# Kernel optimization log

Measured on AMD Instinct MI355X. Metric: run time of the kernel, lower is better.

Reference implementation:

```python
import jax, jax.numpy as jnp
import numpy as np

B, S, D, H = 4, 1024, 1024, 16
DK = D // H
NEG = -1e9


def setup_inputs() -> dict:
    key = jax.random.key(0)
    ks = jax.random.split(key, 8)
    inp = {
        "query": jax.random.normal(ks[0], (B, S, D), dtype=jnp.float32),
        "key": jax.random.normal(ks[1], (B, S, D), dtype=jnp.float32),
        "value": jax.random.normal(ks[2], (B, S, D), dtype=jnp.float32),
        "mask": jax.random.randint(ks[3], (B, S, S), 0, 2, dtype=jnp.int32),
        # bias-free Linear weights, torch layout [out, in]; y = x @ W.T
        "Wq": jax.random.normal(ks[4], (D, D), dtype=jnp.float32) / np.sqrt(D),
        "Wk": jax.random.normal(ks[5], (D, D), dtype=jnp.float32) / np.sqrt(D),
        "Wv": jax.random.normal(ks[6], (D, D), dtype=jnp.float32) / np.sqrt(D),
        "Wo": jax.random.normal(ks[7], (D, D), dtype=jnp.float32) / np.sqrt(D),
    }
    return inp


def _split_heads(x):
    # [B, S, D] -> [B, H, S, DK]
    return x.reshape(B, -1, H, DK).transpose(0, 2, 1, 3)


def reference(query, key, value, mask, Wq, Wk, Wv, Wo):
    q = _split_heads(query @ Wq.T)
    k = _split_heads(key @ Wk.T)
    v = _split_heads(value @ Wv.T)
    scores = jnp.einsum("bhqd,bhkd->bhqk", q, k) / jnp.sqrt(jnp.float32(DK))
    scores = jnp.where(mask[:, None, :, :] == 0, NEG, scores)
    p_attn = jax.nn.softmax(scores, axis=-1)
    x = jnp.einsum("bhqk,bhkd->bhqd", p_attn, v)
    x = x.transpose(0, 2, 1, 3).reshape(B, -1, D)
    # dropout p=0.0 (eval-equivalent): identity
    return x @ Wo.T
```

## Files before the change

### kernel.cpp

```cpp
#include <hip/hip_runtime.h>

#define BB 4
#define SS 1024
#define DD 1024
#define HH 16
#define DKK 64
#define MM (BB*SS)

typedef __bf16 bf16;
typedef __bf16 bf16x8 __attribute__((ext_vector_type(8)));
typedef float f32x4 __attribute__((ext_vector_type(4)));
typedef float f32x16 __attribute__((ext_vector_type(16)));

__device__ __forceinline__ f32x4 mfma16(bf16x8 a, bf16x8 b, f32x4 c) {
  return __builtin_amdgcn_mfma_f32_16x16x32_bf16(a, b, c, 0, 0, 0);
}
__device__ __forceinline__ f32x16 mfma32(bf16x8 a, bf16x8 b, f32x16 c) {
  return __builtin_amdgcn_mfma_f32_32x32x16_bf16(a, b, c, 0, 0, 0);
}
__device__ __forceinline__ float fexp2(float x) {
  return __builtin_amdgcn_exp2f(x);
}
__device__ __forceinline__ void gld_lds16(const bf16* g, bf16* l) {
  __builtin_amdgcn_global_load_lds(
      (const __attribute__((address_space(1))) void*)g,
      (__attribute__((address_space(3))) void*)l, 16, 0, 0);
}

__global__ __launch_bounds__(256)
void k_cvt7(const float* __restrict__ s0, const float* __restrict__ s1,
            const float* __restrict__ s2, const float* __restrict__ s3,
            const float* __restrict__ s4, const float* __restrict__ s5,
            const float* __restrict__ s6,
            bf16* __restrict__ d0, bf16* __restrict__ d1, bf16* __restrict__ d2,
            bf16* __restrict__ d3, bf16* __restrict__ d4, bf16* __restrict__ d5,
            bf16* __restrict__ d6) {
  const int t = blockIdx.y;
  const float* s = (t == 0) ? s0 : (t == 1) ? s1 : (t == 2) ? s2
                 : (t == 3) ? s3 : (t == 4) ? s4 : (t == 5) ? s5 : s6;
  bf16* d = (t == 0) ? d0 : (t == 1) ? d1 : (t == 2) ? d2
          : (t == 3) ? d3 : (t == 4) ? d4 : (t == 5) ? d5 : d6;
  const int n = (t < 3) ? (MM * DD) : (DD * DD);
  const int i0 = (blockIdx.x * 256 + threadIdx.x) * 8;
  if (i0 >= n) return;
  const f32x4 a = *(const f32x4*)(s + i0);
  const f32x4 b = *(const f32x4*)(s + i0 + 4);
  bf16x8 o;
#pragma unroll
  for (int j = 0; j < 4; ++j) { o[j] = (bf16)a[j]; o[4 + j] = (bf16)b[j]; }
  *(bf16x8*)(d + i0) = o;
}

__global__ __launch_bounds__(256) void k_mask_bits(const int* __restrict__ mask,
                                                   unsigned* __restrict__ bits) {
  const int row = blockIdx.x;
  const int b = row >> 10, q = row & 1023;
  const int qblk = q >> 6, qt = (q >> 5) & 1, l = q & 31;
  const size_t base = ((size_t)(b * 16 + qblk) * 2 + qt) * 4;
  const int tid = threadIdx.x;
  const int lane = tid & 63, wv = tid >> 6;
#pragma unroll
  for (int it = 0; it < 4; ++it) {
    const int cb = it * 256 + wv * 64;
    unsigned long long bal = __ballot(mask[(size_t)row * SS + cb + lane] != 0);
    if (lane == 0) {
      const int c0 = cb >> 5;
#pragma unroll
      for (int dd = 0; dd < 2; ++dd) {
        const int c = c0 + dd;
        bits[((base + (c >> 3)) * 8 + (c & 7)) * 32 + l] =
            (unsigned)(bal >> (32 * dd));
      }
    }
  }
}

__global__ __launch_bounds__(256)
void k_kfrag(const bf16* __restrict__ K, bf16* __restrict__ Kf) {
  __shared__ bf16 Kl[32 * 66];
  const int kvb = blockIdx.x, h = blockIdx.y, b = blockIdx.z;
  const int tid = threadIdx.x;
  const int r = tid >> 3, c0 = (tid & 7) * 8;
  *(bf16x8*)&Kl[r * 66 + c0] =
      *(const bf16x8*)(K + (size_t)(b * SS + kvb * 32 + r) * DD + h * 64 + c0);
  __syncthreads();
  const int lane = tid & 63, l31 = lane & 31, hi = lane >> 5;
  const int kt = tid >> 6;
  bf16x8 ok;
#pragma unroll
  for (int j = 0; j < 8; ++j) ok[j] = Kl[l31 * 66 + kt * 16 + hi * 8 + j];
  *(bf16x8*)(Kf + ((size_t)((b * HH + h) * 32 + kvb)) * 2048 + tid * 8) = ok;
}

#define QSCALE 0.1803368801111204f

template<int AF32, int CF32>
__device__ __forceinline__ void gemm_body(const void* __restrict__ Ap,
                                          const float* __restrict__ Wp,
                                          void* __restrict__ Cp,
                                          int Mtot, int N, int K, int blk,
                                          float oscale) {
  __shared__ bf16 Al[128 * 40];
  __shared__ bf16 Bl[128 * 40];
  const int tid = threadIdx.x;
  const int lane = tid & 63;
  const int l15 = lane & 15, l4 = lane >> 4;
  const int wv = tid >> 6;
  const int nbm = Mtot >> 7;
  const int bm = blk % nbm, bn = blk / nbm;
  const size_t m0 = (size_t)bm << 7, n0 = (size_t)bn << 7;
  const int wr = (wv >> 1) << 6, wc = (wv & 1) << 6;
  const int srow = tid >> 2, scol = (tid & 3) << 3;

  f32x4 acc[4][4];
#pragma unroll
  for (int i = 0; i < 4; ++i)
#pragma unroll
    for (int j = 0; j < 4; ++j) acc[i][j] = f32x4{0.f, 0.f, 0.f, 0.f};

  for (int k0 = 0; k0 < K; k0 += 32) {
#pragma unroll
    for (int c = 0; c < 2; ++c) {
      const int row = (c << 6) + srow;
      bf16x8 av;
      if (AF32) {
        const float* s = (const float*)Ap + (m0 + row) * (size_t)K + k0 + scol;
        f32x4 v0 = *(const f32x4*)s;
        f32x4 v1 = *(const f32x4*)(s + 4);
#pragma unroll
        for (int j = 0; j < 4; ++j) { av[j] = (bf16)v0[j]; av[4 + j] = (bf16)v1[j]; }
      } else {
        av = *(const bf16x8*)((const bf16*)Ap + (m0 + row) * (size_t)K + k0 + scol);
      }
      *(bf16x8*)&Al[row * 40 + scol] = av;

      const float* ws_ = Wp + (n0 + row) * (size_t)K + k0 + scol;
      f32x4 w0 = *(const f32x4*)ws_;
      f32x4 w1 = *(const f32x4*)(ws_ + 4);
      bf16x8 wv8;
#pragma unroll
      for (int j = 0; j < 4; ++j) { wv8[j] = (bf16)w0[j]; wv8[4 + j] = (bf16)w1[j]; }
      *(bf16x8*)&Bl[row * 40 + scol] = wv8;
    }
    __syncthreads();

    bf16x8 af[4], bfv[4];
#pragma unroll
    for (int t = 0; t < 4; ++t) {
      af[t]  = *(const bf16x8*)&Al[(wr + t * 16 + l15) * 40 + l4 * 8];
      bfv[t] = *(const bf16x8*)&Bl[(wc + t * 16 + l15) * 40 + l4 * 8];
    }
    __builtin_amdgcn_s_setprio(1);
#pragma unroll
    for (int mt = 0; mt < 4; ++mt)
#pragma unroll
      for (int nt = 0; nt < 4; ++nt)
        acc[mt][nt] = mfma16(af[mt], bfv[nt], acc[mt][nt]);
    __builtin_amdgcn_s_setprio(0);
    __syncthreads();
  }

#pragma unroll
  for (int mt = 0; mt < 4; ++mt)
#pragma unroll
    for (int nt = 0; nt < 4; ++nt)
#pragma unroll
      for (int r = 0; r < 4; ++r) {
        const size_t row = m0 + wr + mt * 16 + l4 * 4 + r;
        const size_t col = n0 + wc + nt * 16 + l15;
        if (CF32) ((float*)Cp)[row * N + col] = acc[mt][nt][r];
        else      ((bf16*)Cp)[row * N + col] = (bf16)(acc[mt][nt][r] * oscale);
      }
}

__global__ __launch_bounds__(256)
void k_gemm_qkv(const float* __restrict__ A0, const float* __restrict__ A1,
                const float* __restrict__ A2, const float* __restrict__ W0,
                const float* __restrict__ W1, const float* __restrict__ W2,
                bf16* __restrict__ C0, bf16* __restrict__ C1, bf16* __restrict__ C2) {
  const int z = blockIdx.z;
  const float* A = (z == 0) ? A0 : (z == 1) ? A1 : A2;
  const float* W = (z == 0) ? W0 : (z == 1) ? W1 : W2;
  bf16* C = (z == 0) ? C0 : (z == 1) ? C1 : C2;
  const float sc = (z == 0) ? QSCALE : 1.0f;
  gemm_body<1, 0>(A, W, C, MM, DD, DD, blockIdx.x, sc);
}

__global__ __launch_bounds__(256)
void k_gemm_out(const bf16* __restrict__ A, const float* __restrict__ W,
                float* __restrict__ C) {
  gemm_body<0, 1>(A, W, C, MM, DD, DD, blockIdx.x, 1.0f);
}

__global__ __launch_bounds__(256)
void k_gemm_qkv_b16(const bf16* __restrict__ A0, const bf16* __restrict__ A1,
                    const bf16* __restrict__ A2, const bf16* __restrict__ W0,
                    const bf16* __restrict__ W1, const bf16* __restrict__ W2,
                    bf16* __restrict__ C0, bf16* __restrict__ C1,
                    bf16* __restrict__ C2) {
  __shared__ bf16 Al[128 * 32];
  __shared__ bf16 Bl[128 * 32];
  const int z = blockIdx.z;
  const bf16* A = (z == 0) ? A0 : (z == 1) ? A1 : A2;
  const bf16* W = (z == 0) ? W0 : (z == 1) ? W1 : W2;
  bf16* C = (z == 0) ? C0 : (z == 1) ? C1 : C2;
  const float oscale = (z == 0) ? QSCALE : 1.0f;

  const int tid = threadIdx.x, lane = tid & 63, w = tid >> 6;
  const int l15 = lane & 15, l4 = lane >> 4;
  const int bm = blockIdx.x & 31, bn = blockIdx.x >> 5;
  const size_t m0 = (size_t)bm << 7, n0 = (size_t)bn << 7;
  const int wr = (w >> 1) << 6, wc = (w & 1) << 6;
  const int srow = w * 32 + (lane >> 2);
  const int scol = (lane & 3) << 3;

  f32x4 acc[4][4];
#pragma unroll
  for (int i = 0; i < 4; ++i)
#pragma unroll
    for (int j = 0; j < 4; ++j) acc[i][j] = f32x4{0.f, 0.f, 0.f, 0.f};

  for (int k0 = 0; k0 < DD; k0 += 32) {
    const bf16* ga = A + (m0 + srow) * (size_t)DD + k0 + scol;
    const bf16* gb = W + (n0 + srow) * (size_t)DD + k0 + scol;
    gld_lds16(ga,            &Al[(w * 32) * 32]);
    gld_lds16(ga + 16 * DD,  &Al[(w * 32 + 16) * 32]);
    gld_lds16(gb,            &Bl[(w * 32) * 32]);
    gld_lds16(gb + 16 * DD,  &Bl[(w * 32 + 16) * 32]);
    __syncthreads();

    bf16x8 af[4], bfv[4];
#pragma unroll
    for (int t = 0; t < 4; ++t) {
      af[t]  = *(const bf16x8*)&Al[(wr + t * 16 + l15) * 32 + l4 * 8];
      bfv[t] = *(const bf16x8*)&Bl[(wc + t * 16 + l15) * 32 + l4 * 8];
    }
#pragma unroll
    for (int mt = 0; mt < 4; ++mt)
#pragma unroll
      for (int nt = 0; nt < 4; ++nt)
        acc[mt][nt] = mfma16(af[mt], bfv[nt], acc[mt][nt]);
    __syncthreads();
  }

#pragma unroll
  for (int mt = 0; mt < 4; ++mt)
#pragma unroll
    for (int nt = 0; nt < 4; ++nt)
#pragma unroll
      for (int r = 0; r < 4; ++r) {
        const size_t row = m0 + wr + mt * 16 + l4 * 4 + r;
        const size_t col = n0 + wc + nt * 16 + l15;
        C[row * DD + col] = (bf16)(acc[mt][nt][r] * oscale);
      }
}

__global__ __launch_bounds__(256)
void k_gemm_out_b16(const bf16* __restrict__ A, const bf16* __restrict__ W,
                    float* __restrict__ C) {
  __shared__ bf16 Al[128 * 32];
  __shared__ bf16 Bl[128 * 32];
  const int tid = threadIdx.x, lane = tid & 63, w = tid >> 6;
  const int l15 = lane & 15, l4 = lane >> 4;
  const int bm = blockIdx.x & 31, bn = blockIdx.x >> 5;
  const size_t m0 = (size_t)bm << 7, n0 = (size_t)bn << 7;
  const int wr = (w >> 1) << 6, wc = (w & 1) << 6;
  const int srow = w * 32 + (lane >> 2);
  const int scol = (lane & 3) << 3;

  f32x4 acc[4][4];
#pragma unroll
  for (int i = 0; i < 4; ++i)
#pragma unroll
    for (int j = 0; j < 4; ++j) acc[i][j] = f32x4{0.f, 0.f, 0.f, 0.f};

  for (int k0 = 0; k0 < DD; k0 += 32) {
    const bf16* ga = A + (m0 + srow) * (size_t)DD + k0 + scol;
    const bf16* gb = W + (n0 + srow) * (size_t)DD + k0 + scol;
    gld_lds16(ga,            &Al[(w * 32) * 32]);
    gld_lds16(ga + 16 * DD,  &Al[(w * 32 + 16) * 32]);
    gld_lds16(gb,            &Bl[(w * 32) * 32]);
    gld_lds16(gb + 16 * DD,  &Bl[(w * 32 + 16) * 32]);
    __syncthreads();

    bf16x8 af[4], bfv[4];
#pragma unroll
    for (int t = 0; t < 4; ++t) {
      af[t]  = *(const bf16x8*)&Al[(wr + t * 16 + l15) * 32 + l4 * 8];
      bfv[t] = *(const bf16x8*)&Bl[(wc + t * 16 + l15) * 32 + l4 * 8];
    }
#pragma unroll
    for (int mt = 0; mt < 4; ++mt)
#pragma unroll
      for (int nt = 0; nt < 4; ++nt)
        acc[mt][nt] = mfma16(af[mt], bfv[nt], acc[mt][nt]);
    __syncthreads();
  }

#pragma unroll
  for (int mt = 0; mt < 4; ++mt)
#pragma unroll
    for (int nt = 0; nt < 4; ++nt)
#pragma unroll
      for (int r = 0; r < 4; ++r) {
        const size_t row = m0 + wr + mt * 16 + l4 * 4 + r;
        const size_t col = n0 + wc + nt * 16 + l15;
        C[row * DD + col] = acc[mt][nt][r];
      }
}

__global__ __launch_bounds__(256)
void k_attn(const bf16* __restrict__ Qw, const bf16* __restrict__ Kf,
            const bf16* __restrict__ Vw, const unsigned* __restrict__ mb,
            bf16* __restrict__ Xw) {
  __shared__ union {
    bf16 v[4][2048];
    struct { float o[64 * 33]; float l[4][64]; float inv[64]; } m;
  } sh;
  const int tid = threadIdx.x, lane = tid & 63, w = tid >> 6;
  const int l31 = lane & 31, hi = lane >> 5;
  const unsigned bid = blockIdx.x;
  const unsigned wg = (bid & 7) * 128 + (bid >> 3);
  const int bh = wg >> 4, qblk = wg & 15;
  const int h = bh & 15, b = bh >> 4;
  const int q0 = qblk * 64;

  bf16x8 qf[2][4];
#pragma unroll
  for (int qt = 0; qt < 2; ++qt) {
    const bf16* Qb = Qw + (size_t)(b * SS + q0 + qt * 32 + l31) * DD + h * 64 + hi * 8;
#pragma unroll
    for (int kt = 0; kt < 4; ++kt) qf[qt][kt] = *(const bf16x8*)(Qb + kt * 16);
  }
  const bf16* Kfb = Kf + ((size_t)((b * HH + h) * 32 + w * 8)) * 2048 + lane * 8;
  const bf16* Vg = Vw + (size_t)(b * SS) * DD + h * 64;
  const unsigned* mq0 = mb +
      ((size_t)(((b * 16 + qblk) * 2 + 0) * 4 + w) * 8) * 32 + l31;
  const unsigned* mq1 = mq0 + 1024;

  const int grow = lane >> 3;
  const int gcol = (lane & 7) * 8;
  const int kvw = w << 8;
  bf16* Vst = sh.v[w];

  f32x16 aco[2][2];
#pragma unroll
  for (int qt = 0; qt < 2; ++qt)
#pragma unroll
    for (int dt = 0; dt < 2; ++dt)
#pragma unroll
      for (int r = 0; r < 16; ++r) aco[qt][dt][r] = 0.f;
  float ssum[2] = { 0.f, 0.f };

  for (int t = 0; t < 8; ++t) {
    const int kv0 = kvw + t * 32;
#pragma unroll
    for (int i_ = 0; i_ < 4; ++i_)
      gld_lds16(Vg + (size_t)(kv0 + i_ * 8 + grow) * DD + gcol, Vst + i_ * 512);
    const bf16* tk = Kfb + t * 2048;
    bf16x8 kf[4];
#pragma unroll
    for (int kt = 0; kt < 4; ++kt) kf[kt] = *(const bf16x8*)(tk + kt * 512);
    const unsigned mw0 = mq0[t * 32], mw1 = mq1[t * 32];

    bf16x8 va[2][2];
    union { bf16x8 v; int q[4]; } pa0[2], pa1[2];

#pragma unroll
    for (int qt = 0; qt < 2; ++qt) {
      f32x16 s;
#pragma unroll
      for (int r = 0; r < 16; ++r) s[r] = 0.f;
      __builtin_amdgcn_s_setprio(1);
#pragma unroll
      for (int kt = 0; kt < 4; ++kt) s = mfma32(kf[kt], qf[qt][kt], s);
      __builtin_amdgcn_s_setprio(0);

      const unsigned mw = qt ? mw1 : mw0;
      float p[16];
#pragma unroll
      for (int r = 0; r < 16; ++r) {
        const int pos = (r & 3) + 8 * (r >> 2) + 4 * hi;
        p[r] = fexp2(((mw >> pos) & 1) ? s[r] : -1e9f);
      }
      {
        float a0 = (p[0] + p[1]) + (p[2] + p[3]);
        float a1 = (p[4] + p[5]) + (p[6] + p[7]);
        float a2 = (p[8] + p[9]) + (p[10] + p[11]);
        float a3 = (p[12] + p[13]) + (p[14] + p[15]);
        ssum[qt] += (a0 + a1) + (a2 + a3);
      }
      int dpk[8];
#pragma unroll
      for (int i = 0; i < 8; ++i) {
        union { bf16 hh[2]; int v; } u;
        u.hh[0] = (bf16)p[2 * i]; u.hh[1] = (bf16)p[2 * i + 1];
        dpk[i] = u.v;
      }
      const int sa = hi ? dpk[0] : dpk[2], sb = hi ? dpk[1] : dpk[3];
      const int sc_ = hi ? dpk[4] : dpk[6], sd = hi ? dpk[5] : dpk[7];
      const int ra = __shfl_xor(sa, 32), rb = __shfl_xor(sb, 32);
      const int rc = __shfl_xor(sc_, 32), rd = __shfl_xor(sd, 32);
      pa0[qt].q[0] = hi ? ra : dpk[0];  pa0[qt].q[1] = hi ? rb : dpk[1];
      pa0[qt].q[2] = hi ? dpk[2] : ra;  pa0[qt].q[3] = hi ? dpk[3] : rb;
      pa1[qt].q[0] = hi ? rc : dpk[4];  pa1[qt].q[1] = hi ? rd : dpk[5];
      pa1[qt].q[2] = hi ? dpk[6] : rc;  pa1[qt].q[3] = hi ? dpk[7] : rd;

      if (qt == 0) {
        asm volatile("s_waitcnt vmcnt(0)" ::: "memory");
        __builtin_amdgcn_sched_barrier(0);
#pragma unroll
        for (int dt = 0; dt < 2; ++dt)
#pragma unroll
          for (int s2 = 0; s2 < 2; ++s2) {
            bf16x8 tv;
#pragma unroll
            for (int j = 0; j < 8; ++j)
              tv[j] = Vst[(s2 * 16 + hi * 8 + j) * 64 + dt * 32 + l31];
            va[dt][s2] = tv;
          }
      }
      __builtin_amdgcn_s_setprio(1);
#pragma unroll
      for (int dt = 0; dt < 2; ++dt) {
        aco[qt][dt] = mfma32(va[dt][0], pa0[qt].v, aco[qt][dt]);
        aco[qt][dt] = mfma32(va[dt][1], pa1[qt].v, aco[qt][dt]);
      }
      __builtin_amdgcn_s_setprio(0);
    }
  }

#pragma unroll
  for (int qt = 0; qt < 2; ++qt) ssum[qt] += __shfl_xor(ssum[qt], 32);
  __syncthreads();
  if (hi == 0) {
#pragma unroll
    for (int qt = 0; qt < 2; ++qt) sh.m.l[w][qt * 32 + l31] = ssum[qt];
  }
  __syncthreads();
  if (w == 0) {
    sh.m.inv[lane] = 1.0f / (sh.m.l[0][lane] + sh.m.l[1][lane] +
                             sh.m.l[2][lane] + sh.m.l[3][lane]);
  }
  __syncthreads();
#pragma unroll
  for (int qt = 0; qt < 2; ++qt) {
    for (int rd2 = 0; rd2 < 4; ++rd2) {
      if (w == rd2) {
#pragma unroll
        for (int dt = 0; dt < 2; ++dt)
#pragma unroll
          for (int r = 0; r < 16; ++r) {
            const int d = dt * 32 + (r & 3) + 8 * (r >> 2) + 4 * hi;
            const int o = d * 33 + l31;
            if (rd2 == 0) sh.m.o[o] = aco[qt][dt][r];
            else          sh.m.o[o] += aco[qt][dt][r];
          }
      }
      __syncthreads();
    }
    {
      const int q = tid >> 3, d0 = (tid & 7) * 8;
      const float inv = sh.m.inv[qt * 32 + q];
      bf16x8 ov;
#pragma unroll
      for (int j = 0; j < 8; ++j) ov[j] = (bf16)(sh.m.o[(d0 + j) * 33 + q] * inv);
      *(bf16x8*)(Xw + (size_t)(b * SS + q0 + qt * 32 + q) * DD + h * 64 + d0) = ov;
    }
    __syncthreads();
  }
}

extern "C" void kernel_launch(void* const* d_in, const int* in_sizes, int n_in,
                              void* d_out, int out_size, void* d_ws, size_t ws_size,
                              hipStream_t stream) {
  const float* q32 = (const float*)d_in[0];
  const float* k32 = (const float*)d_in[1];
  const float* v32 = (const float*)d_in[2];
  const int* mask = (const int*)d_in[3];
  const float* Wq = (const float*)d_in[4];
  const float* Wk = (const float*)d_in[5];
  const float* Wv = (const float*)d_in[6];
  const float* Wo = (const float*)d_in[7];
  float* out = (float*)d_out;

  const size_t eAct = (size_t)MM * DD;
  const size_t eW = (size_t)DD * DD;

  bf16* Qb = (bf16*)d_ws;
  bf16* Kb = Qb + eAct;
  bf16* Vb = Kb + eAct;
  bf16* Xb = Vb + eAct;
  unsigned* mbits = (unsigned*)(Xb + eAct);
  bf16* Kfp = (bf16*)(mbits + (size_t)MM * 32);
  bf16* cvtBase = Kfp + eAct;
  bf16* Aq = cvtBase;
  bf16* Ak = Aq + eAct;
  bf16* Av = Ak + eAct;
  bf16* Wqb = Av + eAct;
  bf16* Wkb = Wqb + eW;
  bf16* Wvb = Wkb + eW;
  bf16* Wob = Wvb + eW;
  const size_t need = (size_t)((bf16*)(Wob + eW) - (bf16*)d_ws) * sizeof(bf16);

  k_mask_bits<<<BB * SS, 256, 0, stream>>>(mask, mbits);
  if (ws_size >= need) {
    k_cvt7<<<dim3(2048, 7), 256, 0, stream>>>(q32, k32, v32, Wq, Wk, Wv, Wo,
                                              Aq, Ak, Av, Wqb, Wkb, Wvb, Wob);
    k_gemm_qkv_b16<<<dim3(256, 1, 3), 256, 0, stream>>>(
        Aq, Ak, Av, Wqb, Wkb, Wvb, Qb, Kb, Vb);
    k_kfrag<<<dim3(32, HH, BB), 256, 0, stream>>>(Kb, Kfp);
    k_attn<<<BB * HH * (SS / 64), 256, 0, stream>>>(Qb, Kfp, Vb, mbits, Xb);
    k_gemm_out_b16<<<256, 256, 0, stream>>>(Xb, Wob, out);
  } else {
    k_gemm_qkv<<<dim3((MM / 128) * (DD / 128), 1, 3), 256, 0, stream>>>(
        q32, k32, v32, Wq, Wk, Wv, Qb, Kb, Vb);
    k_kfrag<<<dim3(32, HH, BB), 256, 0, stream>>>(Kb, Kfp);
    k_attn<<<BB * HH * (SS / 64), 256, 0, stream>>>(Qb, Kfp, Vb, mbits, Xb);
    k_gemm_out<<<(MM / 128) * (DD / 128), 256, 0, stream>>>(Xb, Wo, out);
  }
}
```

Measured before the change: 130.9 us.

## Fuse mask packing into convert, write K fragments from GEMM, prefetch K

Mask-bit packing moves into the fp32-to-bf16 conversion kernel as an extra grid slice. The QKV GEMM now writes K straight into the fragment layout used by attention, which removes the separate k_kfrag kernel and one round trip of K through memory. The attention loop also loads the next tile's K fragments early, between the score MFMAs and the softmax. The cost is fewer launches and less traffic, in exchange for scattered 2-byte stores in the K epilogue and more register pressure from the prefetch.

```diff
diff --git a/kernel.cpp b/kernel.cpp
--- a/kernel.cpp
+++ b/kernel.cpp
@@ -28,27 +28,54 @@
 }
 
 __global__ __launch_bounds__(256)
-void k_cvt7(const float* __restrict__ s0, const float* __restrict__ s1,
+void k_prep(const float* __restrict__ s0, const float* __restrict__ s1,
             const float* __restrict__ s2, const float* __restrict__ s3,
             const float* __restrict__ s4, const float* __restrict__ s5,
             const float* __restrict__ s6,
             bf16* __restrict__ d0, bf16* __restrict__ d1, bf16* __restrict__ d2,
             bf16* __restrict__ d3, bf16* __restrict__ d4, bf16* __restrict__ d5,
-            bf16* __restrict__ d6) {
+            bf16* __restrict__ d6,
+            const int* __restrict__ mask, unsigned* __restrict__ bits) {
   const int t = blockIdx.y;
-  const float* s = (t == 0) ? s0 : (t == 1) ? s1 : (t == 2) ? s2
-                 : (t == 3) ? s3 : (t == 4) ? s4 : (t == 5) ? s5 : s6;
-  bf16* d = (t == 0) ? d0 : (t == 1) ? d1 : (t == 2) ? d2
-          : (t == 3) ? d3 : (t == 4) ? d4 : (t == 5) ? d5 : d6;
-  const int n = (t < 3) ? (MM * DD) : (DD * DD);
-  const int i0 = (blockIdx.x * 256 + threadIdx.x) * 8;
-  if (i0 >= n) return;
-  const f32x4 a = *(const f32x4*)(s + i0);
-  const f32x4 b = *(const f32x4*)(s + i0 + 4);
-  bf16x8 o;
-#pragma unroll
-  for (int j = 0; j < 4; ++j) { o[j] = (bf16)a[j]; o[4 + j] = (bf16)b[j]; }
-  *(bf16x8*)(d + i0) = o;
+  if (t < 7) {
+    const float* s = (t == 0) ? s0 : (t == 1) ? s1 : (t == 2) ? s2
+                   : (t == 3) ? s3 : (t == 4) ? s4 : (t == 5) ? s5 : s6;
+    bf16* d = (t == 0) ? d0 : (t == 1) ? d1 : (t == 2) ? d2
+            : (t == 3) ? d3 : (t == 4) ? d4 : (t == 5) ? d5 : d6;
+    const int n = (t < 3) ? (MM * DD) : (DD * DD);
+    const int i0 = (blockIdx.x * 256 + threadIdx.x) * 8;
+    if (i0 >= n) return;
+    const f32x4 a = *(const f32x4*)(s + i0);
+    const f32x4 bvv = *(const f32x4*)(s + i0 + 4);
+    bf16x8 o;
+#pragma unroll
+    for (int j = 0; j < 4; ++j) { o[j] = (bf16)a[j]; o[4 + j] = (bf16)bvv[j]; }
+    *(bf16x8*)(d + i0) = o;
+    return;
+  }
+  const int tid = threadIdx.x;
+  const int lane = tid & 63, wv = tid >> 6;
+#pragma unroll
+  for (int rr = 0; rr < 2; ++rr) {
+    const int row = blockIdx.x * 2 + rr;
+    const int b = row >> 10, q = row & 1023;
+    const int qblk = q >> 6, qt = (q >> 5) & 1, l = q & 31;
+    const size_t base = ((size_t)(b * 16 + qblk) * 2 + qt) * 4;
+#pragma unroll
+    for (int it = 0; it < 4; ++it) {
+      const int cb = it * 256 + wv * 64;
+      unsigned long long bal = __ballot(mask[(size_t)row * SS + cb + lane] != 0);
+      if (lane == 0) {
+        const int c0 = cb >> 5;
+#pragma unroll
+        for (int dd = 0; dd < 2; ++dd) {
+          const int c = c0 + dd;
+          bits[((base + (c >> 3)) * 8 + (c & 7)) * 32 + l] =
+              (unsigned)(bal >> (32 * dd));
+        }
+      }
+    }
+  }
 }
 
 __global__ __launch_bounds__(256) void k_mask_bits(const int* __restrict__ mask,
@@ -196,14 +223,13 @@
 void k_gemm_qkv_b16(const bf16* __restrict__ A0, const bf16* __restrict__ A1,
                     const bf16* __restrict__ A2, const bf16* __restrict__ W0,
                     const bf16* __restrict__ W1, const bf16* __restrict__ W2,
-                    bf16* __restrict__ C0, bf16* __restrict__ C1,
+                    bf16* __restrict__ C0, bf16* __restrict__ Kf,
                     bf16* __restrict__ C2) {
   __shared__ bf16 Al[128 * 32];
   __shared__ bf16 Bl[128 * 32];
   const int z = blockIdx.z;
   const bf16* A = (z == 0) ? A0 : (z == 1) ? A1 : A2;
   const bf16* W = (z == 0) ? W0 : (z == 1) ? W1 : W2;
-  bf16* C = (z == 0) ? C0 : (z == 1) ? C1 : C2;
   const float oscale = (z == 0) ? QSCALE : 1.0f;
 
   const int tid = threadIdx.x, lane = tid & 63, w = tid >> 6;
@@ -243,16 +269,35 @@
     __syncthreads();
   }
 
-#pragma unroll
-  for (int mt = 0; mt < 4; ++mt)
-#pragma unroll
-    for (int nt = 0; nt < 4; ++nt)
-#pragma unroll
-      for (int r = 0; r < 4; ++r) {
-        const size_t row = m0 + wr + mt * 16 + l4 * 4 + r;
-        const size_t col = n0 + wc + nt * 16 + l15;
-        C[row * DD + col] = (bf16)(acc[mt][nt][r] * oscale);
-      }
+  if (z != 1) {
+    bf16* C = (z == 0) ? C0 : C2;
+#pragma unroll
+    for (int mt = 0; mt < 4; ++mt)
+#pragma unroll
+      for (int nt = 0; nt < 4; ++nt)
+#pragma unroll
+        for (int r = 0; r < 4; ++r) {
+          const size_t row = m0 + wr + mt * 16 + l4 * 4 + r;
+          const size_t col = n0 + wc + nt * 16 + l15;
+          C[row * DD + col] = (bf16)(acc[mt][nt][r] * oscale);
+        }
+  } else {
+#pragma unroll
+    for (int mt = 0; mt < 4; ++mt)
+#pragma unroll
+      for (int nt = 0; nt < 4; ++nt)
+#pragma unroll
+        for (int r = 0; r < 4; ++r) {
+          const int row = (int)m0 + wr + mt * 16 + l4 * 4 + r;
+          const int col = (int)n0 + wc + nt * 16 + l15;
+          const int b = row >> 10, kv = row & 1023;
+          const int kvb = kv >> 5, l31 = kv & 31;
+          const int h = col >> 6, dk = col & 63;
+          const int kt = dk >> 4, hi = (dk >> 3) & 1, j = dk & 7;
+          Kf[((size_t)((b * 16 + h) * 32 + kvb)) * 2048 + kt * 512 +
+             (l31 + 32 * hi) * 8 + j] = (bf16)acc[mt][nt][r];
+        }
+  }
 }
 
 __global__ __launch_bounds__(256)
@@ -352,15 +397,15 @@
       for (int r = 0; r < 16; ++r) aco[qt][dt][r] = 0.f;
   float ssum[2] = { 0.f, 0.f };
 
+  bf16x8 kf[4];
+#pragma unroll
+  for (int kt = 0; kt < 4; ++kt) kf[kt] = *(const bf16x8*)(Kfb + kt * 512);
+
   for (int t = 0; t < 8; ++t) {
     const int kv0 = kvw + t * 32;
 #pragma unroll
     for (int i_ = 0; i_ < 4; ++i_)
       gld_lds16(Vg + (size_t)(kv0 + i_ * 8 + grow) * DD + gcol, Vst + i_ * 512);
-    const bf16* tk = Kfb + t * 2048;
-    bf16x8 kf[4];
-#pragma unroll
-    for (int kt = 0; kt < 4; ++kt) kf[kt] = *(const bf16x8*)(tk + kt * 512);
     const unsigned mw0 = mq0[t * 32], mw1 = mq1[t * 32];
 
     bf16x8 va[2][2];
@@ -375,6 +420,14 @@
 #pragma unroll
       for (int kt = 0; kt < 4; ++kt) s = mfma32(kf[kt], qf[qt][kt], s);
       __builtin_amdgcn_s_setprio(0);
+
+      if (qt == 1 && t < 7) {
+        __builtin_amdgcn_sched_barrier(0);
+        const bf16* tk = Kfb + (t + 1) * 2048;
+#pragma unroll
+        for (int kt = 0; kt < 4; ++kt) kf[kt] = *(const bf16x8*)(tk + kt * 512);
+        __builtin_amdgcn_sched_barrier(0);
+      }
 
       const unsigned mw = qt ? mw1 : mw0;
       float p[16];
@@ -503,16 +556,16 @@
   bf16* Wob = Wvb + eW;
   const size_t need = (size_t)((bf16*)(Wob + eW) - (bf16*)d_ws) * sizeof(bf16);
 
-  k_mask_bits<<<BB * SS, 256, 0, stream>>>(mask, mbits);
   if (ws_size >= need) {
-    k_cvt7<<<dim3(2048, 7), 256, 0, stream>>>(q32, k32, v32, Wq, Wk, Wv, Wo,
-                                              Aq, Ak, Av, Wqb, Wkb, Wvb, Wob);
+    k_prep<<<dim3(2048, 8), 256, 0, stream>>>(q32, k32, v32, Wq, Wk, Wv, Wo,
+                                              Aq, Ak, Av, Wqb, Wkb, Wvb, Wob,
+                                              mask, mbits);
     k_gemm_qkv_b16<<<dim3(256, 1, 3), 256, 0, stream>>>(
-        Aq, Ak, Av, Wqb, Wkb, Wvb, Qb, Kb, Vb);
-    k_kfrag<<<dim3(32, HH, BB), 256, 0, stream>>>(Kb, Kfp);
+        Aq, Ak, Av, Wqb, Wkb, Wvb, Qb, Kfp, Vb);
     k_attn<<<BB * HH * (SS / 64), 256, 0, stream>>>(Qb, Kfp, Vb, mbits, Xb);
     k_gemm_out_b16<<<256, 256, 0, stream>>>(Xb, Wob, out);
   } else {
+    k_mask_bits<<<BB * SS, 256, 0, stream>>>(mask, mbits);
     k_gemm_qkv<<<dim3((MM / 128) * (DD / 128), 1, 3), 256, 0, stream>>>(
         q32, k32, v32, Wq, Wk, Wv, Qb, Kb, Vb);
     k_kfrag<<<dim3(32, HH, BB), 256, 0, stream>>>(Kb, Kfp);
```

New measurement: 128.0 us. 2.3% less time.
